# Performance work log

Measured on AMD Instinct MI355X. Metric: run time of the kernel, lower is better.

## Reference

```python
import jax, jax.numpy as jnp
import numpy as np

N = 50000          # nodes
E = 800000         # edges (before self loops)
H = 4              # attention heads
C = 64             # per-head channels
D_IN = 256
NEG_ATT = 0.2      # GATConv attention LeakyReLU slope
NEG_ACT = 0.01     # nn.LeakyReLU default slope
EPS = 1e-5
MLP_DIMS = [64, 32, 16, 2]


def _gat_layer(x, src, dst, W, a_src, a_dst, b, concat):
    """PyG GATConv: gather -> segment-softmax over dst -> scatter-add."""
    n = x.shape[0]
    h = (x @ W).reshape(n, H, C)                       # [N,H,C]
    s = (h * a_src).sum(-1)                            # [N,H]
    d = (h * a_dst).sum(-1)                            # [N,H]
    e = jax.nn.leaky_relu(s[src] + d[dst], NEG_ATT)    # [E',H]
    m = jax.ops.segment_max(e, dst, num_segments=n)    # per-dst max (self loops -> no empty segs)
    w = jnp.exp(e - m[dst])
    den = jax.ops.segment_sum(w, dst, num_segments=n)
    alpha = w / den[dst]                               # [E',H]
    out = jax.ops.segment_sum(alpha[:, :, None] * h[src], dst, num_segments=n)  # [N,H,C]
    out = out.reshape(n, H * C) if concat else out.mean(axis=1)
    return out + b


def _graph_norm(x, w, b, a):
    mu = x.mean(axis=0, keepdims=True)
    y = x - a * mu
    var = (y * y).mean(axis=0, keepdims=True)
    return w * y * jax.lax.rsqrt(var + EPS) + b


def setup_inputs() -> dict:
    key = jax.random.key(0)
    ks = jax.random.split(key, 40)
    d = {
        'x': jax.random.normal(ks[0], (N, D_IN), dtype=jnp.float32),
        'edge_index': jax.random.randint(ks[1], (2, E), 0, N, dtype=jnp.int64),
    }
    dims_in = [D_IN, H * C, H * C]
    norm_dims = [H * C, H * C, C]
    k = 2
    for i in range(3):
        fan = dims_in[i]
        d[f'W{i}'] = jax.random.normal(ks[k], (fan, H * C), dtype=jnp.float32) / np.sqrt(fan); k += 1
        d[f'as{i}'] = jax.random.normal(ks[k], (H, C), dtype=jnp.float32) / np.sqrt(C); k += 1
        d[f'ad{i}'] = jax.random.normal(ks[k], (H, C), dtype=jnp.float32) / np.sqrt(C); k += 1
        d[f'b{i}'] = jnp.zeros((norm_dims[i],), dtype=jnp.float32)
        d[f'gw{i}'] = jnp.ones((norm_dims[i],), dtype=jnp.float32)
        d[f'gb{i}'] = jnp.zeros((norm_dims[i],), dtype=jnp.float32)
        d[f'ga{i}'] = jnp.ones((norm_dims[i],), dtype=jnp.float32)
    for j in range(3):
        fi, fo = MLP_DIMS[j], MLP_DIMS[j + 1]
        d[f'mW{j}'] = jax.random.normal(ks[k], (fi, fo), dtype=jnp.float32) / np.sqrt(fi); k += 1
        d[f'mb{j}'] = jnp.zeros((fo,), dtype=jnp.float32)
    return d


def reference(x, edge_index,
              W0, as0, ad0, b0, gw0, gb0, ga0,
              W1, as1, ad1, b1, gw1, gb1, ga1,
              W2, as2, ad2, b2, gw2, gb2, ga2,
              mW0, mb0, mW1, mb1, mW2, mb2):
    n = x.shape[0]
    loop = jnp.arange(n, dtype=edge_index.dtype)
    src = jnp.concatenate([edge_index[0], loop])   # add self loops (PyG default)
    dst = jnp.concatenate([edge_index[1], loop])

    h = _gat_layer(x, src, dst, W0, as0, ad0, b0, concat=True)
    h = jax.nn.leaky_relu(_graph_norm(h, gw0, gb0, ga0), NEG_ACT)
    h = _gat_layer(h, src, dst, W1, as1, ad1, b1, concat=True)
    h = jax.nn.leaky_relu(_graph_norm(h, gw1, gb1, ga1), NEG_ACT)
    h = _gat_layer(h, src, dst, W2, as2, ad2, b2, concat=False)
    h = jax.nn.leaky_relu(_graph_norm(h, gw2, gb2, ga2), NEG_ACT)

    h = jax.nn.relu(h @ mW0 + mb0)
    h = jax.nn.relu(h @ mW1 + mb1)
    return h @ mW2 + mb2
```

## Files before the change

kernel.cpp:

```cpp
#include <hip/hip_runtime.h>

#define NN 50000
#define EE 800000
#define ET 850000
#define HH 4
#define CC 64
#define FDIM 256

#define SCAN_BLK 512
#define SCAN_NB ((NN + SCAN_BLK - 1) / SCAN_BLK)

typedef unsigned short ushort;
typedef __bf16 bf16x8 __attribute__((ext_vector_type(8)));
typedef float floatx4 __attribute__((ext_vector_type(4)));
typedef ushort ushort8v __attribute__((ext_vector_type(8)));
struct ushort4s { ushort x, y, z, w; };

__device__ __forceinline__ ushort f2bf(float f) {
  union { float f; unsigned u; } v; v.f = f;
  unsigned r = v.u + 0x7fffu + ((v.u >> 16) & 1u);
  return (ushort)(r >> 16);
}
__device__ __forceinline__ float bf2f(ushort u) {
  return __uint_as_float(((unsigned)u) << 16);
}

__device__ __forceinline__ int get_edge(const void* p, int is64, long long idx) {
  if (is64) return (int)((const long long*)p)[idx];
  return ((const int*)p)[idx];
}

__global__ void detect_kernel(const unsigned int* p, int* flag) {
  __shared__ unsigned red[256];
  int t = threadIdx.x;
  unsigned o = 0;
  for (int i = 0; i < 4; i++) o |= p[(t * 4 + i) * 2 + 1];
  red[t] = o;
  __syncthreads();
  for (int s = 128; s > 0; s >>= 1) {
    if (t < s) red[t] |= red[t + s];
    __syncthreads();
  }
  if (t == 0) *flag = (red[0] == 0) ? 1 : 0;
}

__global__ void degree_kernel(const void* eidx, const int* flag, int* deg) {
  int k = blockIdx.x * blockDim.x + threadIdx.x;
  if (k >= ET) return;
  int is64 = *flag;
  int dst = (k < EE) ? get_edge(eidx, is64, (long long)EE + k) : (k - EE);
  atomicAdd(&deg[dst], 1);
}

__global__ __launch_bounds__(SCAN_BLK) void scan1_kernel(const int* __restrict__ deg,
                                                         int* __restrict__ rowptr,
                                                         int* __restrict__ bsum) {
  __shared__ int sm[SCAN_BLK];
  int t = threadIdx.x;
  int i = blockIdx.x * SCAN_BLK + t;
  int v = (i < NN) ? deg[i] : 0;
  sm[t] = v;
  __syncthreads();
#pragma unroll
  for (int o = 1; o < SCAN_BLK; o <<= 1) {
    int u = (t >= o) ? sm[t - o] : 0;
    __syncthreads();
    sm[t] += u;
    __syncthreads();
  }
  if (i < NN) rowptr[i] = sm[t] - v;
  if (t == SCAN_BLK - 1) bsum[blockIdx.x] = sm[t];
}

__global__ __launch_bounds__(128) void scan2_kernel(const int* __restrict__ bsum,
                                                    int* __restrict__ boff,
                                                    int* __restrict__ rowptr) {
  __shared__ int sm[128];
  int t = threadIdx.x;
  int v = (t < SCAN_NB) ? bsum[t] : 0;
  sm[t] = v;
  __syncthreads();
#pragma unroll
  for (int o = 1; o < 128; o <<= 1) {
    int u = (t >= o) ? sm[t - o] : 0;
    __syncthreads();
    sm[t] += u;
    __syncthreads();
  }
  if (t < SCAN_NB) boff[t] = sm[t] - v;
  if (t == 0) rowptr[NN] = ET;
}

__global__ __launch_bounds__(SCAN_BLK) void scan3_kernel(int* __restrict__ rowptr,
                                                         int* __restrict__ cursor,
                                                         const int* __restrict__ boff) {
  int i = blockIdx.x * SCAN_BLK + threadIdx.x;
  if (i >= NN) return;
  int v = rowptr[i] + boff[blockIdx.x];
  rowptr[i] = v;
  cursor[i] = v;
}

__global__ void fill_kernel(const void* eidx, const int* flag, int* cursor, int* csr_src) {
  int k = blockIdx.x * blockDim.x + threadIdx.x;
  if (k >= ET) return;
  int is64 = *flag;
  int src, dst;
  if (k < EE) {
    src = get_edge(eidx, is64, k);
    dst = get_edge(eidx, is64, (long long)EE + k);
  } else {
    src = dst = k - EE;
  }
  int pos = atomicAdd(&cursor[dst], 1);
  csr_src[pos] = src;
}

__global__ void conv_w_kernel(const float* __restrict__ W0, const float* __restrict__ W1,
                              const float* __restrict__ W2,
                              ushort* __restrict__ T0, ushort* __restrict__ T1,
                              ushort* __restrict__ T2) {
  const float* W = (blockIdx.y == 0) ? W0 : (blockIdx.y == 1) ? W1 : W2;
  ushort* Wt = (blockIdx.y == 0) ? T0 : (blockIdx.y == 1) ? T1 : T2;
  int idx = blockIdx.x * 256 + threadIdx.x;
  int k = idx >> 8, n = idx & 255;
  Wt[n * 256 + k] = f2bf(W[idx]);
}

template <int MODE>
__global__ __launch_bounds__(256) void gemm_bf16(const void* __restrict__ Ap,
                                                 const ushort* __restrict__ Bt,
                                                 ushort* __restrict__ C,
                                                 const float* __restrict__ as_,
                                                 const float* __restrict__ ad_,
                                                 float* __restrict__ s_arr,
                                                 float* __restrict__ d_arr,
                                                 const float* __restrict__ colsum,
                                                 const float* __restrict__ colsumsq,
                                                 const float* __restrict__ ga,
                                                 const float* __restrict__ gw,
                                                 const float* __restrict__ gb) {
  __shared__ ushort As[4 * 512];
  __shared__ ushort Bs[8 * 512];
  __shared__ float scs[FDIM], shs[FDIM];
  int tid = threadIdx.x, w = tid >> 6, l = tid & 63;
  int brow0 = blockIdx.x * 64, bcol0 = blockIdx.y * 128;
  int lm = l & 15, lk = (l >> 4) * 8;
  int arA = min(brow0 + w * 16 + lm, NN - 1);
  size_t arowA = (size_t)arA * 256 + lk;
  const ushort* bg0 = Bt + (size_t)(bcol0 + (2 * w) * 16 + lm) * 256 + lk;
  const ushort* bg1 = Bt + (size_t)(bcol0 + (2 * w + 1) * 16 + lm) * 256 + lk;

  if constexpr (MODE == 1) {
    const float invn = 1.0f / (float)NN;
    float mu = colsum[tid] * invn;
    float ex2 = colsumsq[tid] * invn;
    float a = ga[tid];
    float var = fmaxf(ex2 - (2.f * a - a * a) * mu * mu, 0.f);
    float s = gw[tid] * rsqrtf(var + 1e-5f);
    scs[tid] = s;
    shs[tid] = gb[tid] - s * a * mu;
    __syncthreads();
  }

  floatx4 acc[2][4];
#pragma unroll
  for (int i = 0; i < 2; i++)
#pragma unroll
    for (int j = 0; j < 4; j++) acc[i][j] = floatx4{0.f, 0.f, 0.f, 0.f};

  int wm = (w >> 1) * 2, wn = (w & 1) * 4;

  for (int k0 = 0; k0 < 256; k0 += 32) {
    ushort8v a0;
    if constexpr (MODE == 0) {
      const float* p0 = (const float*)Ap + arowA + k0;
      float4 u0 = *(const float4*)p0, v0 = *(const float4*)(p0 + 4);
      a0 = ushort8v{f2bf(u0.x), f2bf(u0.y), f2bf(u0.z), f2bf(u0.w),
                    f2bf(v0.x), f2bf(v0.y), f2bf(v0.z), f2bf(v0.w)};
    } else {
      ushort8v r0 = *(const ushort8v*)((const ushort*)Ap + arowA + k0);
      int kb = k0 + lk;
#pragma unroll
      for (int j = 0; j < 8; j++) {
        float sc = scs[kb + j], sh = shs[kb + j];
        float y0 = fmaf(sc, bf2f(r0[j]), sh);
        y0 = fmaxf(y0, 0.01f * y0);
        a0[j] = f2bf(y0);
      }
    }
    ushort8v b0 = *(const ushort8v*)(bg0 + k0);
    ushort8v b1 = *(const ushort8v*)(bg1 + k0);
    *(ushort8v*)&As[w * 512 + l * 8] = a0;
    *(ushort8v*)&Bs[(2 * w) * 512 + l * 8] = b0;
    *(ushort8v*)&Bs[(2 * w + 1) * 512 + l * 8] = b1;
    __syncthreads();
    bf16x8 af[2], bfr[4];
#pragma unroll
    for (int i = 0; i < 2; i++) af[i] = *(const bf16x8*)&As[(wm + i) * 512 + l * 8];
#pragma unroll
    for (int j = 0; j < 4; j++) bfr[j] = *(const bf16x8*)&Bs[(wn + j) * 512 + l * 8];
#pragma unroll
    for (int i = 0; i < 2; i++)
#pragma unroll
      for (int j = 0; j < 4; j++)
        acc[i][j] = __builtin_amdgcn_mfma_f32_16x16x32_bf16(af[i], bfr[j], acc[i][j], 0, 0, 0);
    __syncthreads();
  }

  int quad = l >> 4;
#pragma unroll
  for (int i = 0; i < 2; i++) {
    int r0 = brow0 + (wm + i) * 16 + quad * 4;
#pragma unroll
    for (int j = 0; j < 4; j++) {
      int col = bcol0 + (wn + j) * 16 + lm;
#pragma unroll
      for (int r = 0; r < 4; r++) {
        int row = r0 + r;
        if (row < NN) C[(size_t)row * 256 + col] = f2bf(acc[i][j][r]);
      }
    }
  }
  float asv[4], adv[4];
#pragma unroll
  for (int j = 0; j < 4; j++) {
    int col = bcol0 + (wn + j) * 16 + lm;
    asv[j] = as_[col];
    adv[j] = ad_[col];
  }
  int head = (bcol0 >> 6) + (w & 1);
#pragma unroll
  for (int i = 0; i < 2; i++) {
#pragma unroll
    for (int r = 0; r < 4; r++) {
      float sp = acc[i][0][r] * asv[0] + acc[i][1][r] * asv[1] +
                 acc[i][2][r] * asv[2] + acc[i][3][r] * asv[3];
      float dp = acc[i][0][r] * adv[0] + acc[i][1][r] * adv[1] +
                 acc[i][2][r] * adv[2] + acc[i][3][r] * adv[3];
      sp += __shfl_xor(sp, 1); dp += __shfl_xor(dp, 1);
      sp += __shfl_xor(sp, 2); dp += __shfl_xor(dp, 2);
      sp += __shfl_xor(sp, 4); dp += __shfl_xor(dp, 4);
      sp += __shfl_xor(sp, 8); dp += __shfl_xor(dp, 8);
      if (lm == 0) {
        int row = brow0 + (wm + i) * 16 + quad * 4 + r;
        if (row < NN) {
          s_arr[row * HH + head] = sp;
          d_arr[row * HH + head] = dp;
        }
      }
    }
  }
}

template <bool CONCAT>
__global__ __launch_bounds__(256) void agg_kernel(const ushort* __restrict__ hb,
                                                  const float* __restrict__ s_arr,
                                                  const float* __restrict__ d_arr,
                                                  const int* __restrict__ rowptr,
                                                  const int* __restrict__ csr_src,
                                                  const float* __restrict__ bias,
                                                  void* __restrict__ outp) {
  int w = __builtin_amdgcn_readfirstlane(threadIdx.x >> 6);
  int l = threadIdx.x & 63;
  int head = l >> 4;
  int n = blockIdx.x * 4 + w;
  int beg = rowptr[n], end = rowptr[n + 1];
  float dh = d_arr[n * HH + head];
  float a0 = 0.f, a1 = 0.f, a2 = 0.f, a3 = 0.f, den = 0.f;

  int i = beg;
  for (; i + 16 <= end; i += 16) {
    int ss[16];
#pragma unroll
    for (int t = 0; t < 16; t++) ss[t] = csr_src[i + t];
    float ee[16];
#pragma unroll
    for (int t = 0; t < 16; t++) ee[t] = s_arr[ss[t] * HH + head];
    ushort4s hh[16];
#pragma unroll
    for (int t = 0; t < 16; t++)
      hh[t] = *(const ushort4s*)(hb + (unsigned)(ss[t] * FDIM + l * 4));
#pragma unroll
    for (int t = 0; t < 16; t++) {
      float e = ee[t] + dh;
      e = (e > 0.f) ? e : 0.2f * e;
      float wt = __expf(e);
      den += wt;
      a0 = fmaf(wt, bf2f(hh[t].x), a0);
      a1 = fmaf(wt, bf2f(hh[t].y), a1);
      a2 = fmaf(wt, bf2f(hh[t].z), a2);
      a3 = fmaf(wt, bf2f(hh[t].w), a3);
    }
  }
  for (; i + 8 <= end; i += 8) {
    int ss[8];
#pragma unroll
    for (int t = 0; t < 8; t++) ss[t] = csr_src[i + t];
    float ee[8];
#pragma unroll
    for (int t = 0; t < 8; t++) ee[t] = s_arr[ss[t] * HH + head];
    ushort4s hh[8];
#pragma unroll
    for (int t = 0; t < 8; t++)
      hh[t] = *(const ushort4s*)(hb + (unsigned)(ss[t] * FDIM + l * 4));
#pragma unroll
    for (int t = 0; t < 8; t++) {
      float e = ee[t] + dh;
      e = (e > 0.f) ? e : 0.2f * e;
      float wt = __expf(e);
      den += wt;
      a0 = fmaf(wt, bf2f(hh[t].x), a0);
      a1 = fmaf(wt, bf2f(hh[t].y), a1);
      a2 = fmaf(wt, bf2f(hh[t].z), a2);
      a3 = fmaf(wt, bf2f(hh[t].w), a3);
    }
  }
  for (; i + 4 <= end; i += 4) {
    int ss[4];
#pragma unroll
    for (int t = 0; t < 4; t++) ss[t] = csr_src[i + t];
    float ee[4];
#pragma unroll
    for (int t = 0; t < 4; t++) ee[t] = s_arr[ss[t] * HH + head];
    ushort4s hh[4];
#pragma unroll
    for (int t = 0; t < 4; t++)
      hh[t] = *(const ushort4s*)(hb + (unsigned)(ss[t] * FDIM + l * 4));
#pragma unroll
    for (int t = 0; t < 4; t++) {
      float e = ee[t] + dh;
      e = (e > 0.f) ? e : 0.2f * e;
      float wt = __expf(e);
      den += wt;
      a0 = fmaf(wt, bf2f(hh[t].x), a0);
      a1 = fmaf(wt, bf2f(hh[t].y), a1);
      a2 = fmaf(wt, bf2f(hh[t].z), a2);
      a3 = fmaf(wt, bf2f(hh[t].w), a3);
    }
  }
  for (; i < end; i++) {
    int s0 = csr_src[i];
    float e0 = s_arr[s0 * HH + head] + dh;
    ushort4s h0 = *(const ushort4s*)(hb + (unsigned)(s0 * FDIM + l * 4));
    e0 = (e0 > 0.f) ? e0 : 0.2f * e0;
    float w0 = __expf(e0);
    den += w0;
    a0 = fmaf(w0, bf2f(h0.x), a0); a1 = fmaf(w0, bf2f(h0.y), a1);
    a2 = fmaf(w0, bf2f(h0.z), a2); a3 = fmaf(w0, bf2f(h0.w), a3);
  }
  float inv = 1.0f / den;
  float r0 = a0 * inv, r1 = a1 * inv, r2 = a2 * inv, r3 = a3 * inv;

  if (CONCAT) {
    float4 bv = ((const float4*)bias)[l];
    ushort4s o;
    o.x = f2bf(r0 + bv.x); o.y = f2bf(r1 + bv.y);
    o.z = f2bf(r2 + bv.z); o.w = f2bf(r3 + bv.w);
    ((ushort4s*)outp)[(unsigned)(n * 64 + l)] = o;
  } else {
    r0 += __shfl_xor(r0, 16); r1 += __shfl_xor(r1, 16);
    r2 += __shfl_xor(r2, 16); r3 += __shfl_xor(r3, 16);
    r0 += __shfl_xor(r0, 32); r1 += __shfl_xor(r1, 32);
    r2 += __shfl_xor(r2, 32); r3 += __shfl_xor(r3, 32);
    if (l < 16) {
      float4 bv = ((const float4*)bias)[l];
      float4 o;
      o.x = 0.25f * r0 + bv.x; o.y = 0.25f * r1 + bv.y;
      o.z = 0.25f * r2 + bv.z; o.w = 0.25f * r3 + bv.w;
      ((float4*)outp)[(unsigned)(n * 16 + l)] = o;
    }
  }
}

__global__ __launch_bounds__(256) void norm_reduce_bf(const ushort* __restrict__ xin,
                                                      float* colsum, float* colsumsq) {
  __shared__ float4 sm1[256], sm2[256];
  int t = threadIdx.x;
  int c4 = (t & 63) * 4;
  int rl = t >> 6;
  int r0 = blockIdx.x * 128;
  int r1 = min(NN, r0 + 128);
  float s0 = 0.f, s1 = 0.f, s2 = 0.f, s3 = 0.f;
  float q0 = 0.f, q1 = 0.f, q2 = 0.f, q3 = 0.f;
  for (int r = r0 + rl; r < r1; r += 4) {
    ushort4s v = *(const ushort4s*)(xin + (size_t)r * FDIM + c4);
    float f0 = bf2f(v.x), f1 = bf2f(v.y), f2 = bf2f(v.z), f3 = bf2f(v.w);
    s0 += f0; q0 += f0 * f0;
    s1 += f1; q1 += f1 * f1;
    s2 += f2; q2 += f2 * f2;
    s3 += f3; q3 += f3 * f3;
  }
  sm1[t] = float4{s0, s1, s2, s3};
  sm2[t] = float4{q0, q1, q2, q3};
  __syncthreads();
  if (t < 64) {
    float4 a = sm1[t], b = sm1[t + 64], c = sm1[t + 128], d = sm1[t + 192];
    atomicAdd(&colsum[c4 + 0], a.x + b.x + c.x + d.x);
    atomicAdd(&colsum[c4 + 1], a.y + b.y + c.y + d.y);
    atomicAdd(&colsum[c4 + 2], a.z + b.z + c.z + d.z);
    atomicAdd(&colsum[c4 + 3], a.w + b.w + c.w + d.w);
    float4 e = sm2[t], f = sm2[t + 64], g = sm2[t + 128], h = sm2[t + 192];
    atomicAdd(&colsumsq[c4 + 0], e.x + f.x + g.x + h.x);
    atomicAdd(&colsumsq[c4 + 1], e.y + f.y + g.y + h.y);
    atomicAdd(&colsumsq[c4 + 2], e.z + f.z + g.z + h.z);
    atomicAdd(&colsumsq[c4 + 3], e.w + f.w + g.w + h.w);
  }
}

__global__ __launch_bounds__(256) void norm_reduce_f32(const float* __restrict__ xin,
                                                       float* colsum, float* colsumsq) {
  int f = threadIdx.x & (CC - 1);
  int rl = threadIdx.x / CC;
  int r0 = blockIdx.x * 128;
  int r1 = min(NN, r0 + 128);
  float s1 = 0.f, s2 = 0.f;
  for (int r = r0 + rl; r < r1; r += 4) {
    float v = xin[(size_t)r * CC + f];
    s1 += v; s2 += v * v;
  }
  atomicAdd(&colsum[f], s1);
  atomicAdd(&colsumsq[f], s2);
}

__global__ __launch_bounds__(256) void mlp_kernel(const float* __restrict__ xin,
                                                  const float* __restrict__ colsum,
                                                  const float* __restrict__ colsumsq,
                                                  const float* __restrict__ ga,
                                                  const float* __restrict__ gw,
                                                  const float* __restrict__ gb,
                                                  const float* mW0, const float* mb0,
                                                  const float* mW1, const float* mb1,
                                                  const float* mW2, const float* mb2,
                                                  float* __restrict__ out) {
  __shared__ float W0s[64 * 32];
  __shared__ float W1s[32 * 16];
  __shared__ float W2s[16 * 2];
  __shared__ float b0s[32], b1s[16], b2s[2];
  __shared__ float sc[CC], sh[CC];
  int t = threadIdx.x;
  for (int i = t; i < 2048; i += 256) W0s[i] = mW0[i];
  for (int i = t; i < 512; i += 256) W1s[i] = mW1[i];
  if (t < 32) { W2s[t] = mW2[t]; b0s[t] = mb0[t]; }
  if (t < 16) b1s[t] = mb1[t];
  if (t < 2) b2s[t] = mb2[t];
  if (t < CC) {
    const float invn = 1.0f / (float)NN;
    float mu = colsum[t] * invn;
    float ex2 = colsumsq[t] * invn;
    float a = ga[t];
    float var = fmaxf(ex2 - (2.f * a - a * a) * mu * mu, 0.f);
    float s = gw[t] * rsqrtf(var + 1e-5f);
    sc[t] = s; sh[t] = gb[t] - s * a * mu;
  }
  __syncthreads();
  int node = blockIdx.x * 256 + t;
  if (node >= NN) return;
  float in[64];
  const float* xr = xin + (size_t)node * 64;
#pragma unroll
  for (int k = 0; k < 64; k++) {
    float y = sc[k] * xr[k] + sh[k];
    in[k] = (y > 0.f) ? y : 0.01f * y;
  }
  float h1[32];
#pragma unroll
  for (int j = 0; j < 32; j++) h1[j] = b0s[j];
#pragma unroll
  for (int k = 0; k < 64; k++) {
    float v = in[k];
#pragma unroll
    for (int j = 0; j < 32; j++) h1[j] += v * W0s[k * 32 + j];
  }
#pragma unroll
  for (int j = 0; j < 32; j++) h1[j] = fmaxf(h1[j], 0.f);
  float h2[16];
#pragma unroll
  for (int j = 0; j < 16; j++) h2[j] = b1s[j];
#pragma unroll
  for (int k = 0; k < 32; k++) {
    float v = h1[k];
#pragma unroll
    for (int j = 0; j < 16; j++) h2[j] += v * W1s[k * 16 + j];
  }
#pragma unroll
  for (int j = 0; j < 16; j++) h2[j] = fmaxf(h2[j], 0.f);
  float o0 = b2s[0], o1 = b2s[1];
#pragma unroll
  for (int k = 0; k < 16; k++) {
    o0 += h2[k] * W2s[k * 2 + 0];
    o1 += h2[k] * W2s[k * 2 + 1];
  }
  out[(size_t)node * 2 + 0] = o0;
  out[(size_t)node * 2 + 1] = o1;
}

extern "C" void kernel_launch(void* const* d_in, const int* in_sizes, int n_in,
                              void* d_out, int out_size, void* d_ws, size_t ws_size,
                              hipStream_t stream) {
  const float* x = (const float*)d_in[0];
  const void* ei = d_in[1];
  const float* W[3]   = {(const float*)d_in[2],  (const float*)d_in[9],  (const float*)d_in[16]};
  const float* as_[3] = {(const float*)d_in[3],  (const float*)d_in[10], (const float*)d_in[17]};
  const float* ad_[3] = {(const float*)d_in[4],  (const float*)d_in[11], (const float*)d_in[18]};
  const float* b_[3]  = {(const float*)d_in[5],  (const float*)d_in[12], (const float*)d_in[19]};
  const float* gw[3]  = {(const float*)d_in[6],  (const float*)d_in[13], (const float*)d_in[20]};
  const float* gb[3]  = {(const float*)d_in[7],  (const float*)d_in[14], (const float*)d_in[21]};
  const float* ga[3]  = {(const float*)d_in[8],  (const float*)d_in[15], (const float*)d_in[22]};
  const float* mW0 = (const float*)d_in[23];
  const float* mb0 = (const float*)d_in[24];
  const float* mW1 = (const float*)d_in[25];
  const float* mb1 = (const float*)d_in[26];
  const float* mW2 = (const float*)d_in[27];
  const float* mb2 = (const float*)d_in[28];
  float* out = (float*)d_out;

  char* ws = (char*)d_ws;
  size_t off = 0;
  auto take = [&](size_t bytes) -> char* {
    char* p = ws + off;
    off = (off + bytes + 255) & ~(size_t)255;
    return p;
  };
  ushort* hb    = (ushort*)take((size_t)NN * FDIM * 2);
  ushort* aggb  = (ushort*)take((size_t)NN * FDIM * 2);
  float* bufD   = (float*)take((size_t)NN * CC * 4);
  ushort* Wt[3];
  for (int i = 0; i < 3; i++) Wt[i] = (ushort*)take((size_t)256 * 256 * 2);
  float* s_arr  = (float*)take((size_t)NN * HH * 4);
  float* d_arr  = (float*)take((size_t)NN * HH * 4);
  char* zbase   = (char*)take(0);
  int* deg      = (int*)take((size_t)NN * 4);
  float* cs[3];
  for (int i = 0; i < 3; i++) cs[i] = (float*)take(2048);
  size_t zlen   = (size_t)(((char*)cs[2] + 2048) - zbase);
  int* cursor   = (int*)take((size_t)NN * 4);
  int* rowptr   = (int*)take((size_t)(NN + 1) * 4);
  int* csr_src  = (int*)take((size_t)ET * 4);
  int* bsum     = (int*)take(512);
  int* boff     = (int*)take(512);
  int* flag     = (int*)take(256);

  hipMemsetAsync(zbase, 0, zlen, stream);

  detect_kernel<<<1, 256, 0, stream>>>((const unsigned int*)ei, flag);
  degree_kernel<<<(ET + 255) / 256, 256, 0, stream>>>(ei, flag, deg);
  scan1_kernel<<<SCAN_NB, SCAN_BLK, 0, stream>>>(deg, rowptr, bsum);
  scan2_kernel<<<1, 128, 0, stream>>>(bsum, boff, rowptr);
  scan3_kernel<<<SCAN_NB, SCAN_BLK, 0, stream>>>(rowptr, cursor, boff);
  fill_kernel<<<(ET + 255) / 256, 256, 0, stream>>>(ei, flag, cursor, csr_src);

  conv_w_kernel<<<dim3(256, 3), 256, 0, stream>>>(W[0], W[1], W[2], Wt[0], Wt[1], Wt[2]);

  dim3 ggrid((NN + 63) / 64, 2);
  for (int L = 0; L < 3; L++) {
    if (L == 0)
      gemm_bf16<0><<<ggrid, 256, 0, stream>>>((const void*)x, Wt[0], hb,
                                              as_[0], ad_[0], s_arr, d_arr,
                                              nullptr, nullptr, nullptr, nullptr, nullptr);
    else
      gemm_bf16<1><<<ggrid, 256, 0, stream>>>((const void*)aggb, Wt[L], hb,
                                              as_[L], ad_[L], s_arr, d_arr,
                                              cs[L - 1], cs[L - 1] + 256,
                                              ga[L - 1], gw[L - 1], gb[L - 1]);
    if (L < 2) {
      agg_kernel<true><<<NN / 4, 256, 0, stream>>>(hb, s_arr, d_arr, rowptr, csr_src, b_[L], aggb);
      norm_reduce_bf<<<(NN + 127) / 128, 256, 0, stream>>>(aggb, cs[L], cs[L] + 256);
    } else {
      agg_kernel<false><<<NN / 4, 256, 0, stream>>>(hb, s_arr, d_arr, rowptr, csr_src, b_[L], bufD);
      norm_reduce_f32<<<(NN + 127) / 128, 256, 0, stream>>>(bufD, cs[2], cs[2] + 256);
    }
  }
  mlp_kernel<<<(NN + 255) / 256, 256, 0, stream>>>(bufD, cs[2], cs[2] + 256,
                                                   ga[2], gw[2], gb[2],
                                                   mW0, mb0, mW1, mb1, mW2, mb2, out);
}
```

Baseline: 686.2 us.

## Fuse graph-norm stats into aggregation, widen GEMM tile, drop detect kernel

Folds the column sum and sum-of-squares reductions for GraphNorm into the epilogue of the aggregation kernel. Each block atomically adds its partials into one of 32 striped slots to limit atomic contention, and consumers sum the slots. This removes the separate norm_reduce passes that re-read the aggregated features. The GEMM now uses a 32-row by 256-column tile per block with a 1D grid, so each wave covers one full head, and the int64 edge detection moves from a kernel to a host-side check of the input size. Stats now come from pre-rounding fp32 values rather than bf16, which changes the numerics slightly, and the agg kernel gains a __syncthreads and extra atomics.

```diff
diff --git a/kernel.cpp b/kernel.cpp
--- a/kernel.cpp
+++ b/kernel.cpp
@@ -14,6 +14,7 @@
 typedef __bf16 bf16x8 __attribute__((ext_vector_type(8)));
 typedef float floatx4 __attribute__((ext_vector_type(4)));
 typedef ushort ushort8v __attribute__((ext_vector_type(8)));
+typedef ushort ushort4v __attribute__((ext_vector_type(4)));
 struct ushort4s { ushort x, y, z, w; };
 
 __device__ __forceinline__ ushort f2bf(float f) {
@@ -30,24 +31,9 @@
   return ((const int*)p)[idx];
 }
 
-__global__ void detect_kernel(const unsigned int* p, int* flag) {
-  __shared__ unsigned red[256];
-  int t = threadIdx.x;
-  unsigned o = 0;
-  for (int i = 0; i < 4; i++) o |= p[(t * 4 + i) * 2 + 1];
-  red[t] = o;
-  __syncthreads();
-  for (int s = 128; s > 0; s >>= 1) {
-    if (t < s) red[t] |= red[t + s];
-    __syncthreads();
-  }
-  if (t == 0) *flag = (red[0] == 0) ? 1 : 0;
-}
-
-__global__ void degree_kernel(const void* eidx, const int* flag, int* deg) {
+__global__ void degree_kernel(const void* eidx, int is64, int* deg) {
   int k = blockIdx.x * blockDim.x + threadIdx.x;
   if (k >= ET) return;
-  int is64 = *flag;
   int dst = (k < EE) ? get_edge(eidx, is64, (long long)EE + k) : (k - EE);
   atomicAdd(&deg[dst], 1);
 }
@@ -101,10 +87,9 @@
   cursor[i] = v;
 }
 
-__global__ void fill_kernel(const void* eidx, const int* flag, int* cursor, int* csr_src) {
+__global__ void fill_kernel(const void* eidx, int is64, int* cursor, int* csr_src) {
   int k = blockIdx.x * blockDim.x + threadIdx.x;
   if (k >= ET) return;
-  int is64 = *flag;
   int src, dst;
   if (k < EE) {
     src = get_edge(eidx, is64, k);
@@ -135,26 +120,39 @@
                                                  const float* __restrict__ ad_,
                                                  float* __restrict__ s_arr,
                                                  float* __restrict__ d_arr,
-                                                 const float* __restrict__ colsum,
-                                                 const float* __restrict__ colsumsq,
+                                                 const float* __restrict__ statp,
                                                  const float* __restrict__ ga,
                                                  const float* __restrict__ gw,
                                                  const float* __restrict__ gb) {
-  __shared__ ushort As[4 * 512];
-  __shared__ ushort Bs[8 * 512];
+  __shared__ ushort As[2 * 512];
+  __shared__ ushort Bs[16 * 512];
   __shared__ float scs[FDIM], shs[FDIM];
   int tid = threadIdx.x, w = tid >> 6, l = tid & 63;
-  int brow0 = blockIdx.x * 64, bcol0 = blockIdx.y * 128;
+  int brow0 = blockIdx.x * 32;
   int lm = l & 15, lk = (l >> 4) * 8;
-  int arA = min(brow0 + w * 16 + lm, NN - 1);
-  size_t arowA = (size_t)arA * 256 + lk;
-  const ushort* bg0 = Bt + (size_t)(bcol0 + (2 * w) * 16 + lm) * 256 + lk;
-  const ushort* bg1 = Bt + (size_t)(bcol0 + (2 * w + 1) * 16 + lm) * 256 + lk;
+  int s_sub = tid >> 7;
+  int within = tid & 127;
+  int arow = brow0 + s_sub * 16 + ((within >> 1) & 15);
+  arow = min(arow, NN - 1);
+  int kbase = ((within >> 5) << 3) + ((within & 1) << 2);
+  size_t aoff = (size_t)arow * 256 + kbase;
+  int aldst = s_sub * 512 + within * 4;
+  const ushort* bg[4];
+#pragma unroll
+  for (int j = 0; j < 4; j++)
+    bg[j] = Bt + (size_t)((4 * w + j) * 16 + lm) * 256 + lk;
 
   if constexpr (MODE == 1) {
+    float sa = 0.f, sb = 0.f, qa = 0.f, qb = 0.f;
+    for (int k = 0; k < 32; k += 2) {
+      sa += statp[k * 512 + tid];
+      qa += statp[k * 512 + 256 + tid];
+      sb += statp[(k + 1) * 512 + tid];
+      qb += statp[(k + 1) * 512 + 256 + tid];
+    }
     const float invn = 1.0f / (float)NN;
-    float mu = colsum[tid] * invn;
-    float ex2 = colsumsq[tid] * invn;
+    float mu = (sa + sb) * invn;
+    float ex2 = (qa + qb) * invn;
     float a = ga[tid];
     float var = fmaxf(ex2 - (2.f * a - a * a) * mu * mu, 0.f);
     float s = gw[tid] * rsqrtf(var + 1e-5f);
@@ -169,37 +167,36 @@
 #pragma unroll
     for (int j = 0; j < 4; j++) acc[i][j] = floatx4{0.f, 0.f, 0.f, 0.f};
 
-  int wm = (w >> 1) * 2, wn = (w & 1) * 4;
-
   for (int k0 = 0; k0 < 256; k0 += 32) {
-    ushort8v a0;
+    ushort4v av;
     if constexpr (MODE == 0) {
-      const float* p0 = (const float*)Ap + arowA + k0;
-      float4 u0 = *(const float4*)p0, v0 = *(const float4*)(p0 + 4);
-      a0 = ushort8v{f2bf(u0.x), f2bf(u0.y), f2bf(u0.z), f2bf(u0.w),
-                    f2bf(v0.x), f2bf(v0.y), f2bf(v0.z), f2bf(v0.w)};
+      float4 u = *(const float4*)((const float*)Ap + aoff + k0);
+      av = ushort4v{f2bf(u.x), f2bf(u.y), f2bf(u.z), f2bf(u.w)};
     } else {
-      ushort8v r0 = *(const ushort8v*)((const ushort*)Ap + arowA + k0);
-      int kb = k0 + lk;
-#pragma unroll
-      for (int j = 0; j < 8; j++) {
-        float sc = scs[kb + j], sh = shs[kb + j];
-        float y0 = fmaf(sc, bf2f(r0[j]), sh);
-        y0 = fmaxf(y0, 0.01f * y0);
-        a0[j] = f2bf(y0);
+      ushort4v r = *(const ushort4v*)((const ushort*)Ap + aoff + k0);
+      int kb = k0 + kbase;
+#pragma unroll
+      for (int j = 0; j < 4; j++) {
+        float y = fmaf(scs[kb + j], bf2f(r[j]), shs[kb + j]);
+        y = fmaxf(y, 0.01f * y);
+        av[j] = f2bf(y);
       }
     }
-    ushort8v b0 = *(const ushort8v*)(bg0 + k0);
-    ushort8v b1 = *(const ushort8v*)(bg1 + k0);
-    *(ushort8v*)&As[w * 512 + l * 8] = a0;
-    *(ushort8v*)&Bs[(2 * w) * 512 + l * 8] = b0;
-    *(ushort8v*)&Bs[(2 * w + 1) * 512 + l * 8] = b1;
+    ushort8v b0 = *(const ushort8v*)(bg[0] + k0);
+    ushort8v b1 = *(const ushort8v*)(bg[1] + k0);
+    ushort8v b2 = *(const ushort8v*)(bg[2] + k0);
+    ushort8v b3 = *(const ushort8v*)(bg[3] + k0);
+    *(ushort4v*)&As[aldst] = av;
+    *(ushort8v*)&Bs[(4 * w + 0) * 512 + l * 8] = b0;
+    *(ushort8v*)&Bs[(4 * w + 1) * 512 + l * 8] = b1;
+    *(ushort8v*)&Bs[(4 * w + 2) * 512 + l * 8] = b2;
+    *(ushort8v*)&Bs[(4 * w + 3) * 512 + l * 8] = b3;
     __syncthreads();
     bf16x8 af[2], bfr[4];
-#pragma unroll
-    for (int i = 0; i < 2; i++) af[i] = *(const bf16x8*)&As[(wm + i) * 512 + l * 8];
-#pragma unroll
-    for (int j = 0; j < 4; j++) bfr[j] = *(const bf16x8*)&Bs[(wn + j) * 512 + l * 8];
+    af[0] = *(const bf16x8*)&As[l * 8];
+    af[1] = *(const bf16x8*)&As[512 + l * 8];
+#pragma unroll
+    for (int j = 0; j < 4; j++) bfr[j] = *(const bf16x8*)&Bs[(4 * w + j) * 512 + l * 8];
 #pragma unroll
     for (int i = 0; i < 2; i++)
 #pragma unroll
@@ -211,13 +208,13 @@
   int quad = l >> 4;
 #pragma unroll
   for (int i = 0; i < 2; i++) {
-    int r0 = brow0 + (wm + i) * 16 + quad * 4;
+    int rr0 = brow0 + i * 16 + quad * 4;
 #pragma unroll
     for (int j = 0; j < 4; j++) {
-      int col = bcol0 + (wn + j) * 16 + lm;
+      int col = w * 64 + j * 16 + lm;
 #pragma unroll
       for (int r = 0; r < 4; r++) {
-        int row = r0 + r;
+        int row = rr0 + r;
         if (row < NN) C[(size_t)row * 256 + col] = f2bf(acc[i][j][r]);
       }
     }
@@ -225,11 +222,10 @@
   float asv[4], adv[4];
 #pragma unroll
   for (int j = 0; j < 4; j++) {
-    int col = bcol0 + (wn + j) * 16 + lm;
+    int col = w * 64 + j * 16 + lm;
     asv[j] = as_[col];
     adv[j] = ad_[col];
   }
-  int head = (bcol0 >> 6) + (w & 1);
 #pragma unroll
   for (int i = 0; i < 2; i++) {
 #pragma unroll
@@ -243,10 +239,10 @@
       sp += __shfl_xor(sp, 4); dp += __shfl_xor(dp, 4);
       sp += __shfl_xor(sp, 8); dp += __shfl_xor(dp, 8);
       if (lm == 0) {
-        int row = brow0 + (wm + i) * 16 + quad * 4 + r;
+        int row = brow0 + i * 16 + quad * 4 + r;
         if (row < NN) {
-          s_arr[row * HH + head] = sp;
-          d_arr[row * HH + head] = dp;
+          s_arr[row * HH + w] = sp;
+          d_arr[row * HH + w] = dp;
         }
       }
     }
@@ -260,7 +256,10 @@
                                                   const int* __restrict__ rowptr,
                                                   const int* __restrict__ csr_src,
                                                   const float* __restrict__ bias,
-                                                  void* __restrict__ outp) {
+                                                  void* __restrict__ outp,
+                                                  float* __restrict__ statp) {
+  __shared__ float4 ssm[4][64];
+  __shared__ float4 sqm[4][64];
   int w = __builtin_amdgcn_readfirstlane(threadIdx.x >> 6);
   int l = threadIdx.x & 63;
   int head = l >> 4;
@@ -354,10 +353,28 @@
 
   if (CONCAT) {
     float4 bv = ((const float4*)bias)[l];
+    float ox = r0 + bv.x, oy = r1 + bv.y, oz = r2 + bv.z, ow = r3 + bv.w;
     ushort4s o;
-    o.x = f2bf(r0 + bv.x); o.y = f2bf(r1 + bv.y);
-    o.z = f2bf(r2 + bv.z); o.w = f2bf(r3 + bv.w);
+    o.x = f2bf(ox); o.y = f2bf(oy); o.z = f2bf(oz); o.w = f2bf(ow);
     ((ushort4s*)outp)[(unsigned)(n * 64 + l)] = o;
+    ssm[w][l] = float4{ox, oy, oz, ow};
+    sqm[w][l] = float4{ox * ox, oy * oy, oz * oz, ow * ow};
+    __syncthreads();
+    int tid = threadIdx.x;
+    if (tid < 64) {
+      float4 A = ssm[0][tid], B = ssm[1][tid], Cc = ssm[2][tid], D = ssm[3][tid];
+      float* p = statp + (blockIdx.x & 31) * 512 + tid * 4;
+      atomicAdd(p + 0, A.x + B.x + Cc.x + D.x);
+      atomicAdd(p + 1, A.y + B.y + Cc.y + D.y);
+      atomicAdd(p + 2, A.z + B.z + Cc.z + D.z);
+      atomicAdd(p + 3, A.w + B.w + Cc.w + D.w);
+      float4 E = sqm[0][tid], F = sqm[1][tid], G = sqm[2][tid], Hq = sqm[3][tid];
+      float* q = p + 256;
+      atomicAdd(q + 0, E.x + F.x + G.x + Hq.x);
+      atomicAdd(q + 1, E.y + F.y + G.y + Hq.y);
+      atomicAdd(q + 2, E.z + F.z + G.z + Hq.z);
+      atomicAdd(q + 3, E.w + F.w + G.w + Hq.w);
+    }
   } else {
     r0 += __shfl_xor(r0, 16); r1 += __shfl_xor(r1, 16);
     r2 += __shfl_xor(r2, 16); r3 += __shfl_xor(r3, 16);
@@ -369,63 +386,30 @@
       o.x = 0.25f * r0 + bv.x; o.y = 0.25f * r1 + bv.y;
       o.z = 0.25f * r2 + bv.z; o.w = 0.25f * r3 + bv.w;
       ((float4*)outp)[(unsigned)(n * 16 + l)] = o;
-    }
-  }
-}
-
-__global__ __launch_bounds__(256) void norm_reduce_bf(const ushort* __restrict__ xin,
-                                                      float* colsum, float* colsumsq) {
-  __shared__ float4 sm1[256], sm2[256];
-  int t = threadIdx.x;
-  int c4 = (t & 63) * 4;
-  int rl = t >> 6;
-  int r0 = blockIdx.x * 128;
-  int r1 = min(NN, r0 + 128);
-  float s0 = 0.f, s1 = 0.f, s2 = 0.f, s3 = 0.f;
-  float q0 = 0.f, q1 = 0.f, q2 = 0.f, q3 = 0.f;
-  for (int r = r0 + rl; r < r1; r += 4) {
-    ushort4s v = *(const ushort4s*)(xin + (size_t)r * FDIM + c4);
-    float f0 = bf2f(v.x), f1 = bf2f(v.y), f2 = bf2f(v.z), f3 = bf2f(v.w);
-    s0 += f0; q0 += f0 * f0;
-    s1 += f1; q1 += f1 * f1;
-    s2 += f2; q2 += f2 * f2;
-    s3 += f3; q3 += f3 * f3;
-  }
-  sm1[t] = float4{s0, s1, s2, s3};
-  sm2[t] = float4{q0, q1, q2, q3};
-  __syncthreads();
-  if (t < 64) {
-    float4 a = sm1[t], b = sm1[t + 64], c = sm1[t + 128], d = sm1[t + 192];
-    atomicAdd(&colsum[c4 + 0], a.x + b.x + c.x + d.x);
-    atomicAdd(&colsum[c4 + 1], a.y + b.y + c.y + d.y);
-    atomicAdd(&colsum[c4 + 2], a.z + b.z + c.z + d.z);
-    atomicAdd(&colsum[c4 + 3], a.w + b.w + c.w + d.w);
-    float4 e = sm2[t], f = sm2[t + 64], g = sm2[t + 128], h = sm2[t + 192];
-    atomicAdd(&colsumsq[c4 + 0], e.x + f.x + g.x + h.x);
-    atomicAdd(&colsumsq[c4 + 1], e.y + f.y + g.y + h.y);
-    atomicAdd(&colsumsq[c4 + 2], e.z + f.z + g.z + h.z);
-    atomicAdd(&colsumsq[c4 + 3], e.w + f.w + g.w + h.w);
-  }
-}
-
-__global__ __launch_bounds__(256) void norm_reduce_f32(const float* __restrict__ xin,
-                                                       float* colsum, float* colsumsq) {
-  int f = threadIdx.x & (CC - 1);
-  int rl = threadIdx.x / CC;
-  int r0 = blockIdx.x * 128;
-  int r1 = min(NN, r0 + 128);
-  float s1 = 0.f, s2 = 0.f;
-  for (int r = r0 + rl; r < r1; r += 4) {
-    float v = xin[(size_t)r * CC + f];
-    s1 += v; s2 += v * v;
-  }
-  atomicAdd(&colsum[f], s1);
-  atomicAdd(&colsumsq[f], s2);
+      ssm[w][l] = o;
+      sqm[w][l] = float4{o.x * o.x, o.y * o.y, o.z * o.z, o.w * o.w};
+    }
+    __syncthreads();
+    int tid = threadIdx.x;
+    if (tid < 16) {
+      float4 A = ssm[0][tid], B = ssm[1][tid], Cc = ssm[2][tid], D = ssm[3][tid];
+      float* p = statp + (blockIdx.x & 31) * 128 + tid * 4;
+      atomicAdd(p + 0, A.x + B.x + Cc.x + D.x);
+      atomicAdd(p + 1, A.y + B.y + Cc.y + D.y);
+      atomicAdd(p + 2, A.z + B.z + Cc.z + D.z);
+      atomicAdd(p + 3, A.w + B.w + Cc.w + D.w);
+      float4 E = sqm[0][tid], F = sqm[1][tid], G = sqm[2][tid], Hq = sqm[3][tid];
+      float* q = p + 64;
+      atomicAdd(q + 0, E.x + F.x + G.x + Hq.x);
+      atomicAdd(q + 1, E.y + F.y + G.y + Hq.y);
+      atomicAdd(q + 2, E.z + F.z + G.z + Hq.z);
+      atomicAdd(q + 3, E.w + F.w + G.w + Hq.w);
+    }
+  }
 }
 
 __global__ __launch_bounds__(256) void mlp_kernel(const float* __restrict__ xin,
-                                                  const float* __restrict__ colsum,
-                                                  const float* __restrict__ colsumsq,
+                                                  const float* __restrict__ statp,
                                                   const float* __restrict__ ga,
                                                   const float* __restrict__ gw,
                                                   const float* __restrict__ gb,
@@ -445,9 +429,14 @@
   if (t < 16) b1s[t] = mb1[t];
   if (t < 2) b2s[t] = mb2[t];
   if (t < CC) {
+    float s_ = 0.f, q_ = 0.f;
+    for (int k = 0; k < 32; k++) {
+      s_ += statp[k * 128 + t];
+      q_ += statp[k * 128 + 64 + t];
+    }
     const float invn = 1.0f / (float)NN;
-    float mu = colsum[t] * invn;
-    float ex2 = colsumsq[t] * invn;
+    float mu = s_ * invn;
+    float ex2 = q_ * invn;
     float a = ga[t];
     float var = fmaxf(ex2 - (2.f * a - a * a) * mu * mu, 0.f);
     float s = gw[t] * rsqrtf(var + 1e-5f);
@@ -515,6 +504,8 @@
   const float* mb2 = (const float*)d_in[28];
   float* out = (float*)d_out;
 
+  int is64 = (in_sizes[1] == (int)(2u * EE * 8u)) ? 1 : 0;
+
   char* ws = (char*)d_ws;
   size_t off = 0;
   auto take = [&](size_t bytes) -> char* {
@@ -531,47 +522,45 @@
   float* d_arr  = (float*)take((size_t)NN * HH * 4);
   char* zbase   = (char*)take(0);
   int* deg      = (int*)take((size_t)NN * 4);
-  float* cs[3];
-  for (int i = 0; i < 3; i++) cs[i] = (float*)take(2048);
-  size_t zlen   = (size_t)(((char*)cs[2] + 2048) - zbase);
+  float* cs01[2];
+  for (int i = 0; i < 2; i++) cs01[i] = (float*)take(32 * 512 * 4);
+  float* cs2    = (float*)take(32 * 128 * 4);
+  size_t zlen   = (size_t)(((char*)cs2 + 32 * 128 * 4) - zbase);
   int* cursor   = (int*)take((size_t)NN * 4);
   int* rowptr   = (int*)take((size_t)(NN + 1) * 4);
   int* csr_src  = (int*)take((size_t)ET * 4);
   int* bsum     = (int*)take(512);
   int* boff     = (int*)take(512);
-  int* flag     = (int*)take(256);
 
   hipMemsetAsync(zbase, 0, zlen, stream);
 
-  detect_kernel<<<1, 256, 0, stream>>>((const unsigned int*)ei, flag);
-  degree_kernel<<<(ET + 255) / 256, 256, 0, stream>>>(ei, flag, deg);
+  degree_kernel<<<(ET + 255) / 256, 256, 0, stream>>>(ei, is64, deg);
   scan1_kernel<<<SCAN_NB, SCAN_BLK, 0, stream>>>(deg, rowptr, bsum);
   scan2_kernel<<<1, 128, 0, stream>>>(bsum, boff, rowptr);
   scan3_kernel<<<SCAN_NB, SCAN_BLK, 0, stream>>>(rowptr, cursor, boff);
-  fill_kernel<<<(ET + 255) / 256, 256, 0, stream>>>(ei, flag, cursor, csr_src);
+  fill_kernel<<<(ET + 255) / 256, 256, 0, stream>>>(ei, is64, cursor, csr_src);
 
   conv_w_kernel<<<dim3(256, 3), 256, 0, stream>>>(W[0], W[1], W[2], Wt[0], Wt[1], Wt[2]);
 
-  dim3 ggrid((NN + 63) / 64, 2);
+  int ggrid = (NN + 31) / 32;
   for (int L = 0; L < 3; L++) {
     if (L == 0)
       gemm_bf16<0><<<ggrid, 256, 0, stream>>>((const void*)x, Wt[0], hb,
                                               as_[0], ad_[0], s_arr, d_arr,
-                                              nullptr, nullptr, nullptr, nullptr, nullptr);
+                                              nullptr, nullptr, nullptr, nullptr);
     else
       gemm_bf16<1><<<ggrid, 256, 0, stream>>>((const void*)aggb, Wt[L], hb,
                                               as_[L], ad_[L], s_arr, d_arr,
-                                              cs[L - 1], cs[L - 1] + 256,
-                                              ga[L - 1], gw[L - 1], gb[L - 1]);
+                                              cs01[L - 1], ga[L - 1], gw[L - 1], gb[L - 1]);
     if (L < 2) {
-      agg_kernel<true><<<NN / 4, 256, 0, stream>>>(hb, s_arr, d_arr, rowptr, csr_src, b_[L], aggb);
-      norm_reduce_bf<<<(NN + 127) / 128, 256, 0, stream>>>(aggb, cs[L], cs[L] + 256);
+      agg_kernel<true><<<NN / 4, 256, 0, stream>>>(hb, s_arr, d_arr, rowptr, csr_src,
+                                                   b_[L], aggb, cs01[L]);
     } else {
-      agg_kernel<false><<<NN / 4, 256, 0, stream>>>(hb, s_arr, d_arr, rowptr, csr_src, b_[L], bufD);
-      norm_reduce_f32<<<(NN + 127) / 128, 256, 0, stream>>>(bufD, cs[2], cs[2] + 256);
-    }
-  }
-  mlp_kernel<<<(NN + 255) / 256, 256, 0, stream>>>(bufD, cs[2], cs[2] + 256,
+      agg_kernel<false><<<NN / 4, 256, 0, stream>>>(hb, s_arr, d_arr, rowptr, csr_src,
+                                                    b_[L], bufD, cs2);
+    }
+  }
+  mlp_kernel<<<(NN + 255) / 256, 256, 0, stream>>>(bufD, cs2,
                                                    ga[2], gw[2], gb[2],
                                                    mW0, mb0, mW1, mb1, mW2, mb2, out);
 }
```

New measurement: 701.0 us. 2.2% more time.
